# Kernel tuning notes

Measured on AMD Instinct MI355X. Metric: run time of the kernel, lower is better.

Reference implementation:

```python
import jax, jax.numpy as jnp
import numpy as np

N_HEADS = 4


def setup_inputs() -> dict:
    key = jax.random.key(0)
    ks = jax.random.split(key, 8)
    T, B, V, F = 30, 64, 32, 128   # len_pred, batch, n_vehicles, feature_size
    L, LF, TH = 64, 64, 20         # n_lanes, lane_feature_size, len_hist
    vehicles = jax.random.normal(ks[0], (T, B, V, F), dtype=jnp.float32)
    lanes = jax.random.normal(ks[1], (B, V, L, LF), dtype=jnp.float32)
    mask_lanes = jax.random.randint(ks[2], (TH, B, V, L), 0, 2).astype(bool)
    # torch Linear weight layout [out, in]; conv 1x1 weights squeezed to [out, in]
    Wk = jax.random.normal(ks[3], (F, LF), dtype=jnp.float32) / np.sqrt(LF)
    Wv = jax.random.normal(ks[4], (F, LF), dtype=jnp.float32) / np.sqrt(LF)
    Wq = jax.random.normal(ks[5], (F, F), dtype=jnp.float32) / np.sqrt(F)
    Wc = jax.random.normal(ks[6], (F, F), dtype=jnp.float32) / np.sqrt(F)
    return {"vehicles": vehicles, "lanes": lanes, "mask_lanes": mask_lanes,
            "Wk": Wk, "Wv": Wv, "Wq": Wq, "Wc": Wc}


def reference(vehicles, lanes, mask_lanes, Wk, Wv, Wq, Wc):
    # vehicles: [T,B,V,F], lanes: [B,V,L,LF], mask_lanes: [TH,B,V,L] bool
    T, B, V, F = vehicles.shape
    L = lanes.shape[2]
    H = N_HEADS
    hd = F // H
    # Linear projections of lanes (torch Linear: y = x @ W.T)
    k = jnp.einsum('bvlf,gf->bvlg', lanes, Wk).reshape(B, V, L, H, hd)
    v = jnp.einsum('bvlf,gf->bvlg', lanes, Wv).reshape(B, V, L, H, hd)
    # 1x1 Conv2d on feature channels == per-position linear
    q = jnp.einsum('tbvf,gf->tbvg', vehicles, Wq).reshape(T, B, V, H, hd)
    # mask: any over history dim -> [B,V,L] (the second any in attention is a no-op
    # since the mask is repeated identically over T and heads)
    mask = jnp.any(mask_lanes, axis=0)  # [B,V,L]
    scores = jnp.einsum('tbvhd,bvlhd->tbvhl', q, k) / jnp.sqrt(jnp.float32(hd))
    scores = jnp.where(mask[None, :, :, None, :], scores, jnp.float32(-1e9))
    p = jax.nn.softmax(scores, axis=-1)  # [T,B,V,H,L]
    out = jnp.einsum('tbvhl,bvlhd->tbvhd', p, v).reshape(T, B, V, F)
    out = jnp.einsum('tbvf,gf->tbvg', out, Wc) + vehicles
    return out
```

## Files before the change

### kernel.cpp

```cpp
#include <hip/hip_runtime.h>

#define T_  30
#define B_  64
#define V_  32
#define F_  128
#define L_  64
#define LF_ 64
#define TH_ 20
#define H_  4
#define HD_ 32

typedef __attribute__((ext_vector_type(8))) short bf16x8;
typedef __attribute__((ext_vector_type(4))) float f32x4;
#define MFMA(a,b,c) __builtin_amdgcn_mfma_f32_16x16x32_bf16(a, b, c, 0, 0, 0)

__device__ __forceinline__ float bf1(unsigned short u) {
    unsigned int x = ((unsigned int)u) << 16; float f; __builtin_memcpy(&f, &x, 4); return f;
}
__device__ __forceinline__ unsigned short f2bf(float f) {
    unsigned int x; __builtin_memcpy(&x, &f, 4);
    x += 0x7fffu + ((x >> 16) & 1u);
    return (unsigned short)(x >> 16);
}
__device__ __forceinline__ float4 ld4(const void* p, int idx4, bool isBf16) {
    if (isBf16) {
        ushort4 u = ((const ushort4*)p)[idx4];
        return make_float4(bf1(u.x), bf1(u.y), bf1(u.z), bf1(u.w));
    }
    return ((const float4*)p)[idx4];
}
__device__ __forceinline__ void st4bf(unsigned short* p, f32x4 v) {
    ushort4 u = { f2bf(v[0]), f2bf(v[1]), f2bf(v[2]), f2bf(v[3]) };
    *(ushort4*)p = u;
}
__device__ __forceinline__ bf16x8 ldWfrag(const void* W, int off, bool isBf16) {
    if (isBf16) return *(const bf16x8*)((const unsigned short*)W + off);
    const float* p = (const float*)W + off;
    float4 a = *(const float4*)p;
    float4 b = *(const float4*)(p + 4);
    bf16x8 r;
    r[0] = (short)f2bf(a.x); r[1] = (short)f2bf(a.y);
    r[2] = (short)f2bf(a.z); r[3] = (short)f2bf(a.w);
    r[4] = (short)f2bf(b.x); r[5] = (short)f2bf(b.y);
    r[6] = (short)f2bf(b.z); r[7] = (short)f2bf(b.w);
    return r;
}

__global__ __launch_bounds__(512, 4)
void lane_attn_kernel(const void* __restrict__ veh,
                      const void* __restrict__ lanes,
                      const void* __restrict__ maskp,
                      const void* __restrict__ Wk, const void* __restrict__ Wv,
                      const void* __restrict__ Wq, const void* __restrict__ Wc,
                      float* __restrict__ outp)
{
    const int bv    = blockIdx.x;
    const int tid   = threadIdx.x;
    const int w     = tid >> 6;
    const int h     = w >> 1;
    const int shalf = w & 1;
    const int lane  = tid & 63;
    const int quad  = lane >> 4;
    const int lm    = lane & 15;
    const int fbase = h * 32;
    const int fs    = fbase + shalf * 16;

    __shared__ __align__(16) unsigned short sRegion[13824];
    __shared__ __align__(16) unsigned short sK [64 * 136];
    __shared__ __align__(16) unsigned short sVt[128 * 72];
    unsigned short* sQ     = sRegion;
    unsigned short* sO     = sRegion;
    unsigned short* sLanes = sRegion + 4352;
    unsigned short* sVehB  = sRegion + 9472;
    unsigned short* sS     = sRegion + 4352;

    const unsigned short* vh16 = (const unsigned short*)veh;
    const int field = (vh16[2 * lane] >> 7) & 0xFF;
    const bool isBf16 = __popcll(__ballot(field >= 100 && field <= 130)) >= 32;
    const unsigned char* mbp = (const unsigned char*)maskp;
    const bool maskByte = (__ballot(mbp[4 * lane + 1] != 0) != 0ULL);

    bool ok;
    {
        const int* mi = (const int*)maskp;
        int o = 0;
        #pragma unroll
        for (int th = 0; th < TH_; ++th) {
            const size_t e = (size_t)th * (B_ * V_ * L_) + (size_t)bv * L_ + lane;
            o |= maskByte ? (int)mbp[e] : mi[e];
        }
        ok = (o != 0);
    }
    const unsigned long long mok = __ballot(ok);

    bf16x8 wbK[2], wbV[2], wq[4];
    #pragma unroll
    for (int kt = 0; kt < 2; ++kt) {
        const int off = (fs + lm) * 64 + kt * 32 + quad * 8;
        wbK[kt] = ldWfrag(Wk, off, isBf16);
        wbV[kt] = ldWfrag(Wv, off, isBf16);
    }
    #pragma unroll
    for (int kt = 0; kt < 4; ++kt)
        wq[kt] = ldWfrag(Wq, (fs + lm) * 128 + kt * 32 + quad * 8, isBf16);

    for (int u = tid; u < 64 * 16; u += 512) {
        const int l = u >> 4, c4 = u & 15;
        float4 x = ld4(lanes, bv * (L_ * LF_ / 4) + u, isBf16);
        ushort4 y = { f2bf(x.x), f2bf(x.y), f2bf(x.z), f2bf(x.w) };
        *(ushort4*)&sLanes[l * 80 + c4 * 4] = y;
    }
    for (int u = tid; u < 32 * 32; u += 512) {
        const int t = u >> 5, c4 = u & 31;
        ushort4 y = {0, 0, 0, 0};
        if (t < T_) {
            float4 x = ld4(veh, (t * (B_ * V_) + bv) * (F_ / 4) + c4, isBf16);
            y.x = f2bf(x.x); y.y = f2bf(x.y); y.z = f2bf(x.z); y.w = f2bf(x.w);
        }
        *(ushort4*)&sVehB[t * 136 + c4 * 4] = y;
    }
    __syncthreads();

    {
        f32x4 accK[4], accV[4];
        #pragma unroll
        for (int mt = 0; mt < 4; ++mt) { accK[mt] = (f32x4)0.f; accV[mt] = (f32x4)0.f; }
        #pragma unroll
        for (int kt = 0; kt < 2; ++kt) {
            bf16x8 a[4];
            #pragma unroll
            for (int mt = 0; mt < 4; ++mt)
                a[mt] = *(const bf16x8*)&sLanes[(mt * 16 + lm) * 80 + kt * 32 + quad * 8];
            #pragma unroll
            for (int mt = 0; mt < 4; ++mt) {
                accK[mt] = MFMA(a[mt], wbK[kt], accK[mt]);
                accV[mt] = MFMA(a[mt], wbV[kt], accV[mt]);
            }
        }
        const int f = fs + lm;
        #pragma unroll
        for (int mt = 0; mt < 4; ++mt) {
            const int l0 = mt * 16 + quad * 4;
            #pragma unroll
            for (int r = 0; r < 4; ++r) sK[(l0 + r) * 136 + f] = f2bf(accK[mt][r]);
            st4bf(&sVt[f * 72 + l0], accV[mt]);
        }
    }

    {
        f32x4 acc[2];
        acc[0] = (f32x4)0.f; acc[1] = (f32x4)0.f;
        #pragma unroll
        for (int kt = 0; kt < 4; ++kt) {
            bf16x8 a[2];
            #pragma unroll
            for (int mt = 0; mt < 2; ++mt)
                a[mt] = *(const bf16x8*)&sVehB[(mt * 16 + lm) * 136 + kt * 32 + quad * 8];
            #pragma unroll
            for (int mt = 0; mt < 2; ++mt) acc[mt] = MFMA(a[mt], wq[kt], acc[mt]);
        }
        const float sc = 0.17677669529663687f;
        const int g = fs + lm;
        #pragma unroll
        for (int mt = 0; mt < 2; ++mt) {
            const int t0 = mt * 16 + quad * 4;
            #pragma unroll
            for (int r = 0; r < 4; ++r) sQ[(t0 + r) * 136 + g] = f2bf(acc[mt][r] * sc);
        }
    }

    bf16x8 wc[4];
    #pragma unroll
    for (int kt = 0; kt < 4; ++kt)
        wc[kt] = ldWfrag(Wc, (fs + lm) * 128 + kt * 32 + quad * 8, isBf16);

    __syncthreads();

    {
        bf16x8 a[4], b;
        #pragma unroll
        for (int mt = 0; mt < 4; ++mt)
            a[mt] = *(const bf16x8*)&sK[(mt * 16 + lm) * 136 + fbase + quad * 8];
        b = *(const bf16x8*)&sQ[(shalf * 16 + lm) * 136 + fbase + quad * 8];
        const int t = shalf * 16 + lm;
        const bool tok = (t < T_);
        #pragma unroll
        for (int mt = 0; mt < 4; ++mt) {
            f32x4 acc = MFMA(a[mt], b, (f32x4)0.f);
            const int l0 = mt * 16 + quad * 4;
            ushort4 y;
            y.x = f2bf((tok && ((mok >> (l0 + 0)) & 1)) ? __expf(acc[0]) : 0.f);
            y.y = f2bf((tok && ((mok >> (l0 + 1)) & 1)) ? __expf(acc[1]) : 0.f);
            y.z = f2bf((tok && ((mok >> (l0 + 2)) & 1)) ? __expf(acc[2]) : 0.f);
            y.w = f2bf((tok && ((mok >> (l0 + 3)) & 1)) ? __expf(acc[3]) : 0.f);
            *(ushort4*)&sS[(h * 32 + t) * 72 + l0] = y;
        }
    }

    {
        bf16x8 bones;
        #pragma unroll
        for (int j = 0; j < 8; ++j) bones[j] = (short)0x3F80;
        f32x4 acc[2], ssum;
        acc[0] = (f32x4)0.f; acc[1] = (f32x4)0.f; ssum = (f32x4)0.f;
        #pragma unroll
        for (int kt = 0; kt < 2; ++kt) {
            bf16x8 a = *(const bf16x8*)&sS[(h * 32 + shalf * 16 + lm) * 72 + kt * 32 + quad * 8];
            bf16x8 b[2];
            #pragma unroll
            for (int nt = 0; nt < 2; ++nt)
                b[nt] = *(const bf16x8*)&sVt[(fbase + nt * 16 + lm) * 72 + kt * 32 + quad * 8];
            ssum = MFMA(a, bones, ssum);
            #pragma unroll
            for (int nt = 0; nt < 2; ++nt) acc[nt] = MFMA(a, b[nt], acc[nt]);
        }
        #pragma unroll
        for (int r = 0; r < 4; ++r) {
            const float sv = ssum[r];
            const float inv = (sv > 0.f) ? 1.f / sv : 0.f;
            const int t = shalf * 16 + quad * 4 + r;
            #pragma unroll
            for (int nt = 0; nt < 2; ++nt)
                sO[t * 136 + fbase + nt * 16 + lm] = f2bf(acc[nt][r] * inv);
        }
    }

    float res[2][4];
    {
        const int g = fs + lm;
        #pragma unroll
        for (int mt = 0; mt < 2; ++mt)
            #pragma unroll
            for (int r = 0; r < 4; ++r) {
                const int t = mt * 16 + quad * 4 + r;
                float v = 0.f;
                if (t < T_) {
                    const size_t off = ((size_t)t * (B_ * V_) + bv) * F_ + g;
                    v = isBf16 ? bf1(((const unsigned short*)veh)[off])
                               : ((const float*)veh)[off];
                }
                res[mt][r] = v;
            }
    }
    __syncthreads();

    {
        f32x4 acc[2];
        acc[0] = (f32x4)0.f; acc[1] = (f32x4)0.f;
        #pragma unroll
        for (int kt = 0; kt < 4; ++kt) {
            bf16x8 a[2];
            #pragma unroll
            for (int mt = 0; mt < 2; ++mt)
                a[mt] = *(const bf16x8*)&sO[(mt * 16 + lm) * 136 + kt * 32 + quad * 8];
            #pragma unroll
            for (int mt = 0; mt < 2; ++mt) acc[mt] = MFMA(a[mt], wc[kt], acc[mt]);
        }
        const int g = fs + lm;
        #pragma unroll
        for (int mt = 0; mt < 2; ++mt)
            #pragma unroll
            for (int r = 0; r < 4; ++r) {
                const int t = mt * 16 + quad * 4 + r;
                if (t < T_) {
                    const size_t off = ((size_t)t * (B_ * V_) + bv) * F_ + g;
                    outp[off] = acc[mt][r] + res[mt][r];
                }
            }
    }
}

extern "C" void kernel_launch(void* const* d_in, const int* in_sizes, int n_in,
                              void* d_out, int out_size, void* d_ws, size_t ws_size,
                              hipStream_t stream) {
    (void)in_sizes; (void)n_in; (void)out_size; (void)d_ws; (void)ws_size;
    lane_attn_kernel<<<dim3(B_ * V_), dim3(512), 0, stream>>>(
        d_in[0], d_in[1], d_in[2], d_in[3], d_in[4], d_in[5], d_in[6],
        (float*)d_out);
}
```

Baseline: 171.5 us.

## Swap MFMA operand order for row-contiguous outputs and packed bf16 conversions

Swaps the A/B operands of the K, Q, PV and output-projection MFMAs so each lane's four accumulator values are contiguous along the feature dimension. LDS stores become packed 8-byte writes and the final output becomes float4 global stores instead of scalar ones. Hand-written float-to-bf16 rounding is replaced by the packed hardware conversion, and the lanes staging buffer pitch changes from 80 to 88. The residual loads are also vectorised. This cuts instruction count and scattered stores, at the cost of slightly more shared memory and a riskier re-derivation of fragment indexing.

```diff
diff --git a/kernel.cpp b/kernel.cpp
--- a/kernel.cpp
+++ b/kernel.cpp
@@ -1,4 +1,5 @@
 #include <hip/hip_runtime.h>
+#include <hip/hip_bf16.h>
 
 #define T_  30
 #define B_  64
@@ -17,33 +18,21 @@
 __device__ __forceinline__ float bf1(unsigned short u) {
     unsigned int x = ((unsigned int)u) << 16; float f; __builtin_memcpy(&f, &x, 4); return f;
 }
-__device__ __forceinline__ unsigned short f2bf(float f) {
-    unsigned int x; __builtin_memcpy(&x, &f, 4);
-    x += 0x7fffu + ((x >> 16) & 1u);
-    return (unsigned short)(x >> 16);
-}
-__device__ __forceinline__ float4 ld4(const void* p, int idx4, bool isBf16) {
-    if (isBf16) {
-        ushort4 u = ((const ushort4*)p)[idx4];
-        return make_float4(bf1(u.x), bf1(u.y), bf1(u.z), bf1(u.w));
-    }
-    return ((const float4*)p)[idx4];
-}
-__device__ __forceinline__ void st4bf(unsigned short* p, f32x4 v) {
-    ushort4 u = { f2bf(v[0]), f2bf(v[1]), f2bf(v[2]), f2bf(v[3]) };
-    *(ushort4*)p = u;
+__device__ __forceinline__ unsigned int cvtpk(float a, float b) {
+    __hip_bfloat162 h = __float22bfloat162_rn(make_float2(a, b));
+    unsigned int r; __builtin_memcpy(&r, &h, 4); return r;
+}
+__device__ __forceinline__ void st4pk(unsigned short* p, float a, float b, float c, float d) {
+    uint2 u = { cvtpk(a, b), cvtpk(c, d) };
+    *(uint2*)p = u;
 }
 __device__ __forceinline__ bf16x8 ldWfrag(const void* W, int off, bool isBf16) {
     if (isBf16) return *(const bf16x8*)((const unsigned short*)W + off);
     const float* p = (const float*)W + off;
     float4 a = *(const float4*)p;
     float4 b = *(const float4*)(p + 4);
-    bf16x8 r;
-    r[0] = (short)f2bf(a.x); r[1] = (short)f2bf(a.y);
-    r[2] = (short)f2bf(a.z); r[3] = (short)f2bf(a.w);
-    r[4] = (short)f2bf(b.x); r[5] = (short)f2bf(b.y);
-    r[6] = (short)f2bf(b.z); r[7] = (short)f2bf(b.w);
-    return r;
+    uint4 u = { cvtpk(a.x, a.y), cvtpk(a.z, a.w), cvtpk(b.x, b.y), cvtpk(b.z, b.w) };
+    bf16x8 r; __builtin_memcpy(&r, &u, 16); return r;
 }
 
 __global__ __launch_bounds__(512, 4)
@@ -65,13 +54,13 @@
     const int fbase = h * 32;
     const int fs    = fbase + shalf * 16;
 
-    __shared__ __align__(16) unsigned short sRegion[13824];
+    __shared__ __align__(16) unsigned short sRegion[14336];
     __shared__ __align__(16) unsigned short sK [64 * 136];
     __shared__ __align__(16) unsigned short sVt[128 * 72];
     unsigned short* sQ     = sRegion;
     unsigned short* sO     = sRegion;
     unsigned short* sLanes = sRegion + 4352;
-    unsigned short* sVehB  = sRegion + 9472;
+    unsigned short* sVehB  = sRegion + 9984;
     unsigned short* sS     = sRegion + 4352;
 
     const unsigned short* vh16 = (const unsigned short*)veh;
@@ -106,18 +95,29 @@
 
     for (int u = tid; u < 64 * 16; u += 512) {
         const int l = u >> 4, c4 = u & 15;
-        float4 x = ld4(lanes, bv * (L_ * LF_ / 4) + u, isBf16);
-        ushort4 y = { f2bf(x.x), f2bf(x.y), f2bf(x.z), f2bf(x.w) };
-        *(ushort4*)&sLanes[l * 80 + c4 * 4] = y;
+        if (isBf16) {
+            ushort4 x = ((const ushort4*)lanes)[bv * (L_ * LF_ / 4) + u];
+            *(ushort4*)&sLanes[l * 88 + c4 * 4] = x;
+        } else {
+            float4 x = ((const float4*)lanes)[bv * (L_ * LF_ / 4) + u];
+            uint2 y = { cvtpk(x.x, x.y), cvtpk(x.z, x.w) };
+            *(uint2*)&sLanes[l * 88 + c4 * 4] = y;
+        }
     }
     for (int u = tid; u < 32 * 32; u += 512) {
         const int t = u >> 5, c4 = u & 31;
-        ushort4 y = {0, 0, 0, 0};
+        uint2 y = { 0, 0 };
         if (t < T_) {
-            float4 x = ld4(veh, (t * (B_ * V_) + bv) * (F_ / 4) + c4, isBf16);
-            y.x = f2bf(x.x); y.y = f2bf(x.y); y.z = f2bf(x.z); y.w = f2bf(x.w);
-        }
-        *(ushort4*)&sVehB[t * 136 + c4 * 4] = y;
+            const int idx = (t * (B_ * V_) + bv) * (F_ / 4) + c4;
+            if (isBf16) {
+                ushort4 x = ((const ushort4*)veh)[idx];
+                __builtin_memcpy(&y, &x, 8);
+            } else {
+                float4 x = ((const float4*)veh)[idx];
+                y.x = cvtpk(x.x, x.y); y.y = cvtpk(x.z, x.w);
+            }
+        }
+        *(uint2*)&sVehB[t * 136 + c4 * 4] = y;
     }
     __syncthreads();
 
@@ -130,20 +130,19 @@
             bf16x8 a[4];
             #pragma unroll
             for (int mt = 0; mt < 4; ++mt)
-                a[mt] = *(const bf16x8*)&sLanes[(mt * 16 + lm) * 80 + kt * 32 + quad * 8];
+                a[mt] = *(const bf16x8*)&sLanes[(mt * 16 + lm) * 88 + kt * 32 + quad * 8];
             #pragma unroll
             for (int mt = 0; mt < 4; ++mt) {
-                accK[mt] = MFMA(a[mt], wbK[kt], accK[mt]);
+                accK[mt] = MFMA(wbK[kt], a[mt], accK[mt]);
                 accV[mt] = MFMA(a[mt], wbV[kt], accV[mt]);
             }
         }
-        const int f = fs + lm;
         #pragma unroll
         for (int mt = 0; mt < 4; ++mt) {
-            const int l0 = mt * 16 + quad * 4;
-            #pragma unroll
-            for (int r = 0; r < 4; ++r) sK[(l0 + r) * 136 + f] = f2bf(accK[mt][r]);
-            st4bf(&sVt[f * 72 + l0], accV[mt]);
+            st4pk(&sK[(mt * 16 + lm) * 136 + fs + quad * 4],
+                  accK[mt][0], accK[mt][1], accK[mt][2], accK[mt][3]);
+            st4pk(&sVt[(fs + lm) * 72 + mt * 16 + quad * 4],
+                  accV[mt][0], accV[mt][1], accV[mt][2], accV[mt][3]);
         }
     }
 
@@ -152,21 +151,18 @@
         acc[0] = (f32x4)0.f; acc[1] = (f32x4)0.f;
         #pragma unroll
         for (int kt = 0; kt < 4; ++kt) {
-            bf16x8 a[2];
-            #pragma unroll
-            for (int mt = 0; mt < 2; ++mt)
-                a[mt] = *(const bf16x8*)&sVehB[(mt * 16 + lm) * 136 + kt * 32 + quad * 8];
-            #pragma unroll
-            for (int mt = 0; mt < 2; ++mt) acc[mt] = MFMA(a[mt], wq[kt], acc[mt]);
+            bf16x8 b[2];
+            #pragma unroll
+            for (int nt = 0; nt < 2; ++nt)
+                b[nt] = *(const bf16x8*)&sVehB[(nt * 16 + lm) * 136 + kt * 32 + quad * 8];
+            #pragma unroll
+            for (int nt = 0; nt < 2; ++nt) acc[nt] = MFMA(wq[kt], b[nt], acc[nt]);
         }
         const float sc = 0.17677669529663687f;
-        const int g = fs + lm;
-        #pragma unroll
-        for (int mt = 0; mt < 2; ++mt) {
-            const int t0 = mt * 16 + quad * 4;
-            #pragma unroll
-            for (int r = 0; r < 4; ++r) sQ[(t0 + r) * 136 + g] = f2bf(acc[mt][r] * sc);
-        }
+        #pragma unroll
+        for (int nt = 0; nt < 2; ++nt)
+            st4pk(&sQ[(nt * 16 + lm) * 136 + fs + quad * 4],
+                  acc[nt][0] * sc, acc[nt][1] * sc, acc[nt][2] * sc, acc[nt][3] * sc);
     }
 
     bf16x8 wc[4];
@@ -184,16 +180,19 @@
         b = *(const bf16x8*)&sQ[(shalf * 16 + lm) * 136 + fbase + quad * 8];
         const int t = shalf * 16 + lm;
         const bool tok = (t < T_);
+        const unsigned long long msh = (tok ? mok : 0ULL) >> (quad * 4);
+        const unsigned int mlo = (unsigned int)msh, mhi = (unsigned int)(msh >> 32);
         #pragma unroll
         for (int mt = 0; mt < 4; ++mt) {
             f32x4 acc = MFMA(a[mt], b, (f32x4)0.f);
-            const int l0 = mt * 16 + quad * 4;
-            ushort4 y;
-            y.x = f2bf((tok && ((mok >> (l0 + 0)) & 1)) ? __expf(acc[0]) : 0.f);
-            y.y = f2bf((tok && ((mok >> (l0 + 1)) & 1)) ? __expf(acc[1]) : 0.f);
-            y.z = f2bf((tok && ((mok >> (l0 + 2)) & 1)) ? __expf(acc[2]) : 0.f);
-            y.w = f2bf((tok && ((mok >> (l0 + 3)) & 1)) ? __expf(acc[3]) : 0.f);
-            *(ushort4*)&sS[(h * 32 + t) * 72 + l0] = y;
+            const unsigned int mw = (mt >= 2) ? mhi : mlo;
+            const int bp = (mt * 16) & 31;
+            float e0 = ((mw >> (bp + 0)) & 1u) ? __expf(acc[0]) : 0.f;
+            float e1 = ((mw >> (bp + 1)) & 1u) ? __expf(acc[1]) : 0.f;
+            float e2 = ((mw >> (bp + 2)) & 1u) ? __expf(acc[2]) : 0.f;
+            float e3 = ((mw >> (bp + 3)) & 1u) ? __expf(acc[3]) : 0.f;
+            uint2 y = { cvtpk(e0, e1), cvtpk(e2, e3) };
+            *(uint2*)&sS[(h * 32 + t) * 72 + mt * 16 + quad * 4] = y;
         }
     }
 
@@ -205,42 +204,38 @@
         acc[0] = (f32x4)0.f; acc[1] = (f32x4)0.f; ssum = (f32x4)0.f;
         #pragma unroll
         for (int kt = 0; kt < 2; ++kt) {
-            bf16x8 a = *(const bf16x8*)&sS[(h * 32 + shalf * 16 + lm) * 72 + kt * 32 + quad * 8];
-            bf16x8 b[2];
-            #pragma unroll
-            for (int nt = 0; nt < 2; ++nt)
-                b[nt] = *(const bf16x8*)&sVt[(fbase + nt * 16 + lm) * 72 + kt * 32 + quad * 8];
-            ssum = MFMA(a, bones, ssum);
-            #pragma unroll
-            for (int nt = 0; nt < 2; ++nt) acc[nt] = MFMA(a, b[nt], acc[nt]);
-        }
-        #pragma unroll
-        for (int r = 0; r < 4; ++r) {
-            const float sv = ssum[r];
-            const float inv = (sv > 0.f) ? 1.f / sv : 0.f;
-            const int t = shalf * 16 + quad * 4 + r;
-            #pragma unroll
-            for (int nt = 0; nt < 2; ++nt)
-                sO[t * 136 + fbase + nt * 16 + lm] = f2bf(acc[nt][r] * inv);
-        }
-    }
-
-    float res[2][4];
-    {
-        const int g = fs + lm;
+            bf16x8 bp = *(const bf16x8*)&sS[(h * 32 + shalf * 16 + lm) * 72 + kt * 32 + quad * 8];
+            bf16x8 av[2];
+            #pragma unroll
+            for (int mt = 0; mt < 2; ++mt)
+                av[mt] = *(const bf16x8*)&sVt[(fbase + mt * 16 + lm) * 72 + kt * 32 + quad * 8];
+            ssum = MFMA(bones, bp, ssum);
+            #pragma unroll
+            for (int mt = 0; mt < 2; ++mt) acc[mt] = MFMA(av[mt], bp, acc[mt]);
+        }
+        const float sv  = ssum[0];
+        const float inv = (sv > 0.f) ? 1.f / sv : 0.f;
+        const int t = shalf * 16 + lm;
         #pragma unroll
         for (int mt = 0; mt < 2; ++mt)
-            #pragma unroll
-            for (int r = 0; r < 4; ++r) {
-                const int t = mt * 16 + quad * 4 + r;
-                float v = 0.f;
-                if (t < T_) {
-                    const size_t off = ((size_t)t * (B_ * V_) + bv) * F_ + g;
-                    v = isBf16 ? bf1(((const unsigned short*)veh)[off])
-                               : ((const float*)veh)[off];
-                }
-                res[mt][r] = v;
-            }
+            st4pk(&sO[t * 136 + fbase + mt * 16 + quad * 4],
+                  acc[mt][0] * inv, acc[mt][1] * inv, acc[mt][2] * inv, acc[mt][3] * inv);
+    }
+
+    float4 res[2];
+    #pragma unroll
+    for (int nt = 0; nt < 2; ++nt) {
+        const int t = nt * 16 + lm;
+        res[nt] = make_float4(0.f, 0.f, 0.f, 0.f);
+        if (t < T_) {
+            const size_t off = ((size_t)t * (B_ * V_) + bv) * F_ + fs + quad * 4;
+            if (isBf16) {
+                ushort4 u = *(const ushort4*)((const unsigned short*)veh + off);
+                res[nt] = make_float4(bf1(u.x), bf1(u.y), bf1(u.z), bf1(u.w));
+            } else {
+                res[nt] = *(const float4*)((const float*)veh + off);
+            }
+        }
     }
     __syncthreads();
 
@@ -249,24 +244,23 @@
         acc[0] = (f32x4)0.f; acc[1] = (f32x4)0.f;
         #pragma unroll
         for (int kt = 0; kt < 4; ++kt) {
-            bf16x8 a[2];
-            #pragma unroll
-            for (int mt = 0; mt < 2; ++mt)
-                a[mt] = *(const bf16x8*)&sO[(mt * 16 + lm) * 136 + kt * 32 + quad * 8];
-            #pragma unroll
-            for (int mt = 0; mt < 2; ++mt) acc[mt] = MFMA(a[mt], wc[kt], acc[mt]);
-        }
-        const int g = fs + lm;
-        #pragma unroll
-        for (int mt = 0; mt < 2; ++mt)
-            #pragma unroll
-            for (int r = 0; r < 4; ++r) {
-                const int t = mt * 16 + quad * 4 + r;
-                if (t < T_) {
-                    const size_t off = ((size_t)t * (B_ * V_) + bv) * F_ + g;
-                    outp[off] = acc[mt][r] + res[mt][r];
-                }
-            }
+            bf16x8 b[2];
+            #pragma unroll
+            for (int nt = 0; nt < 2; ++nt)
+                b[nt] = *(const bf16x8*)&sO[(nt * 16 + lm) * 136 + kt * 32 + quad * 8];
+            #pragma unroll
+            for (int nt = 0; nt < 2; ++nt) acc[nt] = MFMA(wc[kt], b[nt], acc[nt]);
+        }
+        #pragma unroll
+        for (int nt = 0; nt < 2; ++nt) {
+            const int t = nt * 16 + lm;
+            if (t < T_) {
+                const size_t off = ((size_t)t * (B_ * V_) + bv) * F_ + fs + quad * 4;
+                float4 o = make_float4(acc[nt][0] + res[nt].x, acc[nt][1] + res[nt].y,
+                                       acc[nt][2] + res[nt].z, acc[nt][3] + res[nt].w);
+                *(float4*)&outp[off] = o;
+            }
+        }
     }
 }
 
```

Measured after the change: 172.4 us. No clear change (+0.6%).
